# Kernel optimization log

Hardware: AMD Instinct MI355X
Metric: run time of the kernel (lower is better)

## Reference

```python
import jax, jax.numpy as jnp
import numpy as np

N, L, C, KF = 32, 1024, 3, 256
H = C * KF            # hidden_dim = 768
M = 3072              # mlp_dim
EPS = 1e-6


def setup_inputs() -> dict:
    key = jax.random.key(0)
    ks = jax.random.split(key, 14)
    s = lambda fan: 1.0 / np.sqrt(fan)
    return {
        "x": jax.random.normal(ks[0], (N, L, H), dtype=jnp.float32),
        # per-channel QKV linears: Linear(k_factor, 3*k_factor) for each channel
        "W_qkv": jax.random.normal(ks[1], (C, KF, 3 * KF), dtype=jnp.float32) * s(KF),
        "b_qkv": jax.random.normal(ks[2], (C, 3 * KF), dtype=jnp.float32) * 0.01,
        "W_out": jax.random.normal(ks[3], (KF, KF), dtype=jnp.float32) * s(KF),
        "b_out": jax.random.normal(ks[4], (KF,), dtype=jnp.float32) * 0.01,
        "ln1_g": jnp.ones((H,), jnp.float32),
        "ln1_b": jnp.zeros((H,), jnp.float32),
        "ln2_g": jnp.ones((H,), jnp.float32),
        "ln2_b": jnp.zeros((H,), jnp.float32),
        "W1": jax.random.normal(ks[5], (H, M), dtype=jnp.float32) * s(H),
        "b1": jax.random.normal(ks[6], (M,), dtype=jnp.float32) * 1e-6,
        "W2": jax.random.normal(ks[7], (M, H), dtype=jnp.float32) * s(M),
        "b2": jax.random.normal(ks[8], (H,), dtype=jnp.float32) * 1e-6,
    }


def _ln(x, g, b):
    mu = jnp.mean(x, axis=-1, keepdims=True)
    var = jnp.mean(jnp.square(x - mu), axis=-1, keepdims=True)
    return (x - mu) * jax.lax.rsqrt(var + EPS) * g + b


def _criss_cross_attn(h, W_qkv, b_qkv, W_out, b_out):
    # h: [N, L, H]; hidden layout is channel-major: (C, KF)
    hc = h.reshape(h.shape[0], h.shape[1], C, KF)
    qkv = jnp.einsum("nlck,ckd->nlcd", hc, W_qkv) + b_qkv      # [N,L,C,3KF]
    q, k, v = jnp.split(qkv, 3, axis=-1)                        # each [N,L,C,KF]
    # move k_factor axis before channel axis: [N,L,KF,C]
    q = jnp.swapaxes(q, -1, -2)
    k = jnp.swapaxes(k, -1, -2)
    v = jnp.swapaxes(v, -1, -2)
    # outer-product scores over channels: [N,L,KF,C,C]
    scores = q[..., :, None] * k[..., None, :] / np.sqrt(KF)
    attn = jax.nn.softmax(scores, axis=-1)
    # einsum 'ijklm,ijkl->ijkm': sum over first channel axis
    ctx = jnp.einsum("nlkcd,nlkc->nlkd", attn, v)               # [N,L,KF,C]
    ctx = jnp.swapaxes(ctx, -1, -2)                             # [N,L,C,KF]
    out = ctx @ W_out + b_out                                   # fc_out per k_factor
    return out.reshape(h.shape[0], h.shape[1], H)


def reference(x, W_qkv, b_qkv, W_out, b_out, ln1_g, ln1_b, ln2_g, ln2_b, W1, b1, W2, b2):
    h = _ln(x, ln1_g, ln1_b)
    a = _criss_cross_attn(h, W_qkv, b_qkv, W_out, b_out)
    xr = a + x                                                   # residual (dropout=0)
    y = _ln(xr, ln2_g, ln2_b)
    y = jax.nn.gelu(y @ W1 + b1, approximate=False) @ W2 + b2    # MLPBlock
    return xr + y
```

## Files before the change

### kernel.cpp

```cpp
#include <hip/hip_runtime.h>
#include <hip/hip_bf16.h>
#include <math.h>

typedef __attribute__((ext_vector_type(8))) short short8;
typedef __attribute__((ext_vector_type(4))) float f32x4;

__device__ __forceinline__ float bf2f(__hip_bfloat16 h) { return __bfloat162float(h); }
__device__ __forceinline__ __hip_bfloat16 f2bf(float f) { return __float2bfloat16(f); }

__device__ __forceinline__ float gelu_f(float v) {
  const float u = v * (0.7978845608f + 0.0356774081f * v * v);
  const float e = __expf(2.0f * u);
  const float t = 1.0f - 2.0f * __builtin_amdgcn_rcpf(e + 1.0f);
  return 0.5f * v * (1.0f + t);
}

__global__ __launch_bounds__(256) void ln_kernel(
    const float* __restrict__ in, const float* __restrict__ g,
    const float* __restrict__ b, __hip_bfloat16* __restrict__ out)
{
  __shared__ float sm1[4], sm2[4];
  const int row = blockIdx.x;
  const int tid = threadIdx.x;
  const float* p = in + (size_t)row * 768;
  float x0 = p[tid], x1 = p[tid + 256], x2 = p[tid + 512];
  float s = x0 + x1 + x2;
  #pragma unroll
  for (int off = 32; off > 0; off >>= 1) s += __shfl_down(s, off, 64);
  const int l = tid & 63, w = tid >> 6;
  if (l == 0) sm1[w] = s;
  __syncthreads();
  const float mu = (sm1[0] + sm1[1] + sm1[2] + sm1[3]) * (1.0f / 768.0f);
  const float d0 = x0 - mu, d1 = x1 - mu, d2 = x2 - mu;
  float ss = d0*d0 + d1*d1 + d2*d2;
  #pragma unroll
  for (int off = 32; off > 0; off >>= 1) ss += __shfl_down(ss, off, 64);
  if (l == 0) sm2[w] = ss;
  __syncthreads();
  const float var = (sm2[0] + sm2[1] + sm2[2] + sm2[3]) * (1.0f / 768.0f);
  const float rstd = rsqrtf(var + 1e-6f);
  __hip_bfloat16* q = out + (size_t)row * 768;
  q[tid]       = f2bf(d0 * rstd * g[tid]       + b[tid]);
  q[tid + 256] = f2bf(d1 * rstd * g[tid + 256] + b[tid + 256]);
  q[tid + 512] = f2bf(d2 * rstd * g[tid + 512] + b[tid + 512]);
}

__global__ __launch_bounds__(256) void attn_kernel(
    const __hip_bfloat162* __restrict__ qkv, __hip_bfloat162* __restrict__ ctx)
{
  const long t = (long)blockIdx.x * 256 + threadIdx.x;
  const long row = t >> 7;
  const int kp = (int)(t & 127);
  const __hip_bfloat162* p = qkv + row * 1152;
  float q[3][2], k[3][2], v[3][2];
  #pragma unroll
  for (int c = 0; c < 3; ++c) {
    __hip_bfloat162 qq = p[c*384 + kp];
    __hip_bfloat162 kk = p[c*384 + 128 + kp];
    __hip_bfloat162 vv = p[c*384 + 256 + kp];
    q[c][0] = __low2float(qq); q[c][1] = __high2float(qq);
    k[c][0] = __low2float(kk); k[c][1] = __high2float(kk);
    v[c][0] = __low2float(vv); v[c][1] = __high2float(vv);
  }
  float o[3][2] = {};
  #pragma unroll
  for (int u = 0; u < 2; ++u) {
    #pragma unroll
    for (int c = 0; c < 3; ++c) {
      const float s0 = q[c][u]*k[0][u]*0.0625f, s1 = q[c][u]*k[1][u]*0.0625f, s2 = q[c][u]*k[2][u]*0.0625f;
      const float m = fmaxf(s0, fmaxf(s1, s2));
      const float e0 = __expf(s0-m), e1 = __expf(s1-m), e2 = __expf(s2-m);
      const float inv = v[c][u] / (e0 + e1 + e2);
      o[0][u] += e0*inv; o[1][u] += e1*inv; o[2][u] += e2*inv;
    }
  }
  __hip_bfloat162* po = ctx + row * 384;
  #pragma unroll
  for (int d = 0; d < 3; ++d)
    po[d*128 + kp] = __hip_bfloat162{f2bf(o[d][0]), f2bf(o[d][1])};
}

__global__ __launch_bounds__(256) void transpose_bf16_kernel(
    const float* __restrict__ in, __hip_bfloat16* __restrict__ out, int K, int N)
{
  __shared__ float tile[32][33];
  in  += (size_t)blockIdx.z * K * N;
  out += (size_t)blockIdx.z * K * N;
  const int n0 = blockIdx.x * 32;
  const int k0 = blockIdx.y * 32;
  const int tx = threadIdx.x & 31, ty = threadIdx.x >> 5;
  #pragma unroll
  for (int r = 0; r < 32; r += 8)
    tile[ty + r][tx] = in[(size_t)(k0 + ty + r) * N + n0 + tx];
  __syncthreads();
  #pragma unroll
  for (int r = 0; r < 32; r += 8)
    out[(size_t)(n0 + ty + r) * K + k0 + tx] = f2bf(tile[tx][ty + r]);
}

#define BM 128
#define BN 128
#define BK 32

template<int MODE>
__global__ __launch_bounds__(256) void gemm_bt_kernel(
    const __hip_bfloat16* __restrict__ A, int lda, long strideA,
    const __hip_bfloat16* __restrict__ Bt, int ldb, long strideB,
    float* __restrict__ Cf, __hip_bfloat16* __restrict__ Cb, int ldc, long strideC,
    const float* __restrict__ bias, long strideBias,
    const float* __restrict__ res,
    int K)
{
  __shared__ __align__(16) char sAll[2 * 16384];

  const int z = blockIdx.z;
  A    += (size_t)z * strideA;
  Bt   += (size_t)z * strideB;
  bias += (size_t)z * strideBias;
  const long cOff = (long)z * strideC;

  const long tileM = (long)blockIdx.x * BM;
  const int  tileN = blockIdx.y * BN;

  const int tid  = threadIdx.x;
  const int lane = tid & 63;
  const int wv   = tid >> 6;
  const int waveM = (wv & 1) * 64;
  const int waveN = (wv >> 1) * 64;

  const int srow  = tid >> 2;
  const int selem = ((tid & 3) ^ ((srow >> 1) & 3)) * 8;
  const int frow = lane & 15;
  const int fkb  = (((lane >> 4) ^ ((frow >> 1) & 3)) << 4);

  const __hip_bfloat16* Ab = A  + tileM * (size_t)lda + selem;
  const __hip_bfloat16* Bb = Bt + (long)tileN * (size_t)ldb + selem;

  f32x4 acc[4][4] = {};

  const int T = K / BK;

  {
    #pragma unroll
    for (int hh = 0; hh < 2; ++hh) {
      const int r = hh * 64 + srow;
      __builtin_amdgcn_global_load_lds(
          (const __attribute__((address_space(1))) void*)(Ab + (size_t)r * lda),
          (__attribute__((address_space(3))) void*)(sAll + hh*4096 + tid*16), 16, 0, 0);
      __builtin_amdgcn_global_load_lds(
          (const __attribute__((address_space(1))) void*)(Bb + (size_t)r * ldb),
          (__attribute__((address_space(3))) void*)(sAll + 8192 + hh*4096 + tid*16), 16, 0, 0);
    }
  }

  for (int t = 0; t < T; ++t) {
    const int buf = (t & 1) * 16384;
    if (t + 1 < T) {
      const int nbuf = 16384 - buf;
      const int k0 = (t + 1) * BK;
      #pragma unroll
      for (int hh = 0; hh < 2; ++hh) {
        const int r = hh * 64 + srow;
        __builtin_amdgcn_global_load_lds(
            (const __attribute__((address_space(1))) void*)(Ab + (size_t)r * lda + k0),
            (__attribute__((address_space(3))) void*)(sAll + nbuf + hh*4096 + tid*16), 16, 0, 0);
        __builtin_amdgcn_global_load_lds(
            (const __attribute__((address_space(1))) void*)(Bb + (size_t)r * ldb + k0),
            (__attribute__((address_space(3))) void*)(sAll + nbuf + 8192 + hh*4096 + tid*16), 16, 0, 0);
      }
      asm volatile("s_waitcnt vmcnt(4)" ::: "memory");
    } else {
      asm volatile("s_waitcnt vmcnt(0)" ::: "memory");
    }
    __builtin_amdgcn_s_barrier();
    asm volatile("" ::: "memory");

    const char* sAb = sAll + buf;
    const char* sBb = sAb + 8192;
    short8 aF[4], bF[4];
    #pragma unroll
    for (int i = 0; i < 4; ++i)
      aF[i] = *(const short8*)(sAb + (waveM + i*16 + frow) * 64 + fkb);
    #pragma unroll
    for (int j = 0; j < 4; ++j)
      bF[j] = *(const short8*)(sBb + (waveN + j*16 + frow) * 64 + fkb);
    #pragma unroll
    for (int i = 0; i < 4; ++i)
      #pragma unroll
      for (int j = 0; j < 4; ++j)
        acc[i][j] = __builtin_amdgcn_mfma_f32_16x16x32_bf16(aF[i], bF[j], acc[i][j], 0, 0, 0);

    __builtin_amdgcn_s_barrier();
  }

  #pragma unroll
  for (int i = 0; i < 4; ++i) {
    const long row0 = tileM + waveM + i*16 + ((lane >> 4) * 4);
    #pragma unroll
    for (int j = 0; j < 4; ++j) {
      const int col = tileN + waveN + j*16 + (lane & 15);
      const float bv = bias[col];
      #pragma unroll
      for (int r = 0; r < 4; ++r) {
        const long idx = cOff + (row0 + r) * (long)ldc + col;
        const float v = acc[i][j][r] + bv;
        if (MODE == 0) {
          Cb[idx] = f2bf(v);
        } else if (MODE == 1 || MODE == 3) {
          Cf[idx] = v + res[idx];
        } else {
          Cb[idx] = f2bf(gelu_f(v));
        }
      }
    }
  }
}

#define GLL16(src, dst) __builtin_amdgcn_global_load_lds( \
    (const __attribute__((address_space(1))) void*)(src), \
    (__attribute__((address_space(3))) void*)(dst), 16, 0, 0)

#define STAGE_TILE3(bb, koff) do { \
    char* bse = sAll + (bb) * 49152; \
    GLL16(Ab + (size_t)(0*64) * lda + (koff), bse + 0*8192  + tid*16); \
    GLL16(Ab + (size_t)(1*64) * lda + (koff), bse + 1*8192  + tid*16); \
    GLL16(Ab + (size_t)(2*64) * lda + (koff), bse + 2*8192  + tid*16); \
    GLL16(Ab + (size_t)(3*64) * lda + (koff), bse + 3*8192  + tid*16); \
    GLL16(Bb + (size_t)(0*64) * ldb + (koff), bse + 32768 + 0*8192 + tid*16); \
    GLL16(Bb + (size_t)(1*64) * ldb + (koff), bse + 32768 + 1*8192 + tid*16); \
  } while (0)

template<int MODE>
__global__ __launch_bounds__(512, 2) void gemm3_kernel(
    const __hip_bfloat16* __restrict__ A, int lda, long strideA,
    const __hip_bfloat16* __restrict__ Bt, int ldb, long strideB,
    float* __restrict__ Cf, __hip_bfloat16* __restrict__ Cb, int ldc, long strideC,
    const float* __restrict__ bias, long strideBias,
    const float* __restrict__ res,
    int K)
{
  __shared__ __align__(16) char sAll[3 * 49152];

  const int z = blockIdx.z;
  A    += (size_t)z * strideA;
  Bt   += (size_t)z * strideB;
  bias += (size_t)z * strideBias;
  const long cOff = (long)z * strideC;

  const long tileM = (long)blockIdx.x * 256;
  const int  tileN = blockIdx.y * 128;

  const int tid  = threadIdx.x;
  const int lane = tid & 63;
  const int wv   = tid >> 6;
  const int wm   = wv & 3;
  const int wn   = wv >> 2;

  const int srow  = tid >> 3;
  const int selem = ((tid & 7) ^ (srow & 7)) * 8;

  const __hip_bfloat16* Ab = A  + (tileM + srow) * (size_t)lda + selem;
  const __hip_bfloat16* Bb = Bt + ((long)tileN + srow) * (size_t)ldb + selem;

  const int fk   = lane >> 4;
  const int fx   = lane & 7;
  const int frow = lane & 15;
  const int arow = (wm*64 + frow) * 128;
  const int brow = 32768 + (wn*64 + frow) * 128;
  const int ax0  = ((0*4 + fk) ^ fx) * 16;
  const int ax1  = ((1*4 + fk) ^ fx) * 16;

  f32x4 acc[4][4] = {};
  const int T = K / 64;

  STAGE_TILE3(0, 0);
  STAGE_TILE3(1, (T > 1 ? 1 : 0) * 64);

  int bcur = 0;
  for (int t = 0; t < T; ++t) {
    const char* base = sAll + bcur * 49152;
    const int bstg = (bcur == 0) ? 2 : (bcur - 1);
    const int kn   = (t + 2 < T ? t + 2 : T - 1) * 64;

    asm volatile("s_waitcnt vmcnt(6)" ::: "memory");
    __builtin_amdgcn_s_barrier();
    asm volatile("" ::: "memory");

    STAGE_TILE3(bstg, kn);

    short8 aF0[4], bF0[4], aF1[4], bF1[4];
    #pragma unroll
    for (int i = 0; i < 4; ++i) aF0[i] = *(const short8*)(base + arow + i*2048 + ax0);
    #pragma unroll
    for (int j = 0; j < 4; ++j) bF0[j] = *(const short8*)(base + brow + j*2048 + ax0);
    #pragma unroll
    for (int i = 0; i < 4; ++i) aF1[i] = *(const short8*)(base + arow + i*2048 + ax1);
    #pragma unroll
    for (int j = 0; j < 4; ++j) bF1[j] = *(const short8*)(base + brow + j*2048 + ax1);

    asm volatile("s_waitcnt lgkmcnt(8)" ::: "memory");
    __builtin_amdgcn_sched_barrier(0);
    __builtin_amdgcn_s_setprio(1);
    #pragma unroll
    for (int i = 0; i < 4; ++i)
      #pragma unroll
      for (int j = 0; j < 4; ++j)
        acc[i][j] = __builtin_amdgcn_mfma_f32_16x16x32_bf16(aF0[i], bF0[j], acc[i][j], 0, 0, 0);
    __builtin_amdgcn_s_setprio(0);

    asm volatile("s_waitcnt lgkmcnt(0)" ::: "memory");
    __builtin_amdgcn_sched_barrier(0);
    __builtin_amdgcn_s_setprio(1);
    #pragma unroll
    for (int i = 0; i < 4; ++i)
      #pragma unroll
      for (int j = 0; j < 4; ++j)
        acc[i][j] = __builtin_amdgcn_mfma_f32_16x16x32_bf16(aF1[i], bF1[j], acc[i][j], 0, 0, 0);
    __builtin_amdgcn_s_setprio(0);

    bcur = (bcur == 2) ? 0 : (bcur + 1);
  }

  asm volatile("s_waitcnt vmcnt(0)" ::: "memory");

  #pragma unroll
  for (int i = 0; i < 4; ++i) {
    const long row0 = tileM + wm*64 + i*16 + ((lane >> 4) * 4);
    #pragma unroll
    for (int j = 0; j < 4; ++j) {
      const int col = tileN + wn*64 + j*16 + (lane & 15);
      const float bv = bias[col];
      #pragma unroll
      for (int r = 0; r < 4; ++r) {
        const long idx = cOff + (row0 + r) * (long)ldc + col;
        const float v = acc[i][j][r] + bv;
        if (MODE == 0) {
          Cb[idx] = f2bf(v);
        } else if (MODE == 1 || MODE == 3) {
          Cf[idx] = v + res[idx];
        } else {
          Cb[idx] = f2bf(gelu_f(v));
        }
      }
    }
  }
}

extern "C" void kernel_launch(void* const* d_in, const int* in_sizes, int n_in,
                              void* d_out, int out_size, void* d_ws, size_t ws_size,
                              hipStream_t stream)
{
  const float* x     = (const float*)d_in[0];
  const float* W_qkv = (const float*)d_in[1];
  const float* b_qkv = (const float*)d_in[2];
  const float* W_out = (const float*)d_in[3];
  const float* b_out = (const float*)d_in[4];
  const float* ln1_g = (const float*)d_in[5];
  const float* ln1_b = (const float*)d_in[6];
  const float* ln2_g = (const float*)d_in[7];
  const float* ln2_b = (const float*)d_in[8];
  const float* W1    = (const float*)d_in[9];
  const float* b1    = (const float*)d_in[10];
  const float* W2    = (const float*)d_in[11];
  const float* b2    = (const float*)d_in[12];
  float* out = (float*)d_out;

  char* ws = (char*)d_ws;
  __hip_bfloat16* h     = (__hip_bfloat16*)(ws + 0);
  __hip_bfloat16* qkv   = (__hip_bfloat16*)(ws + 50331648);
  __hip_bfloat16* ctx   = (__hip_bfloat16*)(ws + 0);
  __hip_bfloat16* act   = (__hip_bfloat16*)(ws + 0);
  __hip_bfloat16* yln   = (__hip_bfloat16*)(ws + 201326592);
  __hip_bfloat16* wqkvT = (__hip_bfloat16*)(ws + 251658240);
  __hip_bfloat16* woutT = (__hip_bfloat16*)(ws + 252837888);
  __hip_bfloat16* w1T   = (__hip_bfloat16*)(ws + 252968960);
  __hip_bfloat16* w2T   = (__hip_bfloat16*)(ws + 257687552);

  transpose_bf16_kernel<<<dim3(768/32, 256/32, 3), 256, 0, stream>>>(W_qkv, wqkvT, 256, 768);
  transpose_bf16_kernel<<<dim3(256/32, 256/32, 1), 256, 0, stream>>>(W_out, woutT, 256, 256);
  transpose_bf16_kernel<<<dim3(3072/32, 768/32, 1), 256, 0, stream>>>(W1, w1T, 768, 3072);
  transpose_bf16_kernel<<<dim3(768/32, 3072/32, 1), 256, 0, stream>>>(W2, w2T, 3072, 768);

  ln_kernel<<<32768, 256, 0, stream>>>(x, ln1_g, ln1_b, h);

  gemm3_kernel<0><<<dim3(32768/256, 768/128, 3), 512, 0, stream>>>(
      h, 768, 256, wqkvT, 256, 768*256, nullptr, qkv, 2304, 768, b_qkv, 768, nullptr, 256);

  attn_kernel<<<16384, 256, 0, stream>>>((const __hip_bfloat162*)qkv, (__hip_bfloat162*)ctx);

  gemm_bt_kernel<1><<<dim3(98304/BM, 256/BN, 1), 256, 0, stream>>>(
      ctx, 256, 0, woutT, 256, 0, out, nullptr, 256, 0, b_out, 0, x, 256);

  ln_kernel<<<32768, 256, 0, stream>>>(out, ln2_g, ln2_b, yln);

  gemm3_kernel<2><<<dim3(32768/256, 3072/128, 1), 512, 0, stream>>>(
      yln, 768, 0, w1T, 768, 0, nullptr, act, 3072, 0, b1, 0, nullptr, 768);

  gemm3_kernel<3><<<dim3(32768/256, 768/128, 1), 512, 0, stream>>>(
      act, 3072, 0, w2T, 3072, 0, out, nullptr, 768, 0, b2, 0, out, 3072);
}
```

Baseline: 855.5 us.

## Load B fragments directly to registers and enlarge GEMM tile to 256x256

Replaces the 256x128 GEMM with a 256x256-tile kernel. Only A goes through a triple-buffered LDS pipeline; each wave loads its B fragments straight from global memory into double-buffered registers one k-step ahead. The aim is to halve A re-reads across N tiles and to drop LDS traffic for B. In exchange, register use (accumulators plus two B buffers) rises sharply at 2 blocks per CU, the grid shrinks (e.g. only 384 blocks for the 768-wide GEMMs), and uncoalesced direct global B loads may expose latency. The main loop steps two k-tiles per iteration, so odd T would overrun.

```diff
diff --git a/kernel.cpp b/kernel.cpp
--- a/kernel.cpp
+++ b/kernel.cpp
@@ -220,18 +220,76 @@
     (const __attribute__((address_space(1))) void*)(src), \
     (__attribute__((address_space(3))) void*)(dst), 16, 0, 0)
 
-#define STAGE_TILE3(bb, koff) do { \
-    char* bse = sAll + (bb) * 49152; \
-    GLL16(Ab + (size_t)(0*64) * lda + (koff), bse + 0*8192  + tid*16); \
-    GLL16(Ab + (size_t)(1*64) * lda + (koff), bse + 1*8192  + tid*16); \
-    GLL16(Ab + (size_t)(2*64) * lda + (koff), bse + 2*8192  + tid*16); \
-    GLL16(Ab + (size_t)(3*64) * lda + (koff), bse + 3*8192  + tid*16); \
-    GLL16(Bb + (size_t)(0*64) * ldb + (koff), bse + 32768 + 0*8192 + tid*16); \
-    GLL16(Bb + (size_t)(1*64) * ldb + (koff), bse + 32768 + 1*8192 + tid*16); \
+#define STAGE_A3(bb, koff) do { \
+    char* bse = sA3 + (bb) * 32768; \
+    GLL16(Ab + (size_t)(0*64) * lda + (koff), bse + 0*8192 + tid*16); \
+    GLL16(Ab + (size_t)(1*64) * lda + (koff), bse + 1*8192 + tid*16); \
+    GLL16(Ab + (size_t)(2*64) * lda + (koff), bse + 2*8192 + tid*16); \
+    GLL16(Ab + (size_t)(3*64) * lda + (koff), bse + 3*8192 + tid*16); \
   } while (0)
 
+#define LOADB_ALL(dst, kt) do { \
+    _Pragma("unroll") \
+    for (int jh_ = 0; jh_ < 2; ++jh_) \
+      _Pragma("unroll") \
+      for (int j_ = 0; j_ < 2; ++j_) \
+        _Pragma("unroll") \
+        for (int kk_ = 0; kk_ < 2; ++kk_) \
+          dst[jh_][j_][kk_] = *(const short8*)(Bb + (size_t)(jh_*128 + j_*16) * ldb + (kt)*64 + kk_*32); \
+  } while (0)
+
+#define GBODY(t_, bufi, BCUR, BNXT, stg) do { \
+    const char* base = sA3 + (bufi) * 32768; \
+    asm volatile("s_waitcnt vmcnt(4)" ::: "memory");      \
+    __builtin_amdgcn_s_barrier();                         \
+    asm volatile("" ::: "memory"); \
+    short8 aF[4][2]; \
+    _Pragma("unroll") \
+    for (int i_ = 0; i_ < 4; ++i_) { \
+      aF[i_][0] = *(const short8*)(base + arow + i_*2048 + ax0); \
+      aF[i_][1] = *(const short8*)(base + arow + i_*2048 + ax1); \
+    } \
+    { const int ktn = ((t_) + 1 < T ? (t_) + 1 : T - 1); \
+      LOADB_ALL(BNXT, ktn); } \
+    __builtin_amdgcn_sched_barrier(0);                    \
+    { const int kts = ((t_) + 2 < T ? (t_) + 2 : T - 1); \
+      STAGE_A3(stg, kts * 64); } \
+    __builtin_amdgcn_sched_barrier(0); \
+    asm volatile("s_waitcnt lgkmcnt(0)" ::: "memory");    \
+    __builtin_amdgcn_sched_barrier(0); \
+    __builtin_amdgcn_s_setprio(1); \
+    _Pragma("unroll") \
+    for (int i_ = 0; i_ < 4; ++i_) \
+      _Pragma("unroll") \
+      for (int jh_ = 0; jh_ < 2; ++jh_) \
+        _Pragma("unroll") \
+        for (int j_ = 0; j_ < 2; ++j_) { \
+          acc[0][jh_][i_][j_] = __builtin_amdgcn_mfma_f32_16x16x32_bf16(aF[i_][0], BCUR[jh_][j_][0], acc[0][jh_][i_][j_], 0, 0, 0); \
+          acc[0][jh_][i_][j_] = __builtin_amdgcn_mfma_f32_16x16x32_bf16(aF[i_][1], BCUR[jh_][j_][1], acc[0][jh_][i_][j_], 0, 0, 0); \
+        } \
+    __builtin_amdgcn_s_setprio(0); \
+    _Pragma("unroll") \
+    for (int i_ = 0; i_ < 4; ++i_) { \
+      aF[i_][0] = *(const short8*)(base + 16384 + arow + i_*2048 + ax0); \
+      aF[i_][1] = *(const short8*)(base + 16384 + arow + i_*2048 + ax1); \
+    } \
+    asm volatile("s_waitcnt lgkmcnt(0)" ::: "memory");    \
+    __builtin_amdgcn_sched_barrier(0); \
+    __builtin_amdgcn_s_setprio(1); \
+    _Pragma("unroll") \
+    for (int i_ = 0; i_ < 4; ++i_) \
+      _Pragma("unroll") \
+      for (int jh_ = 0; jh_ < 2; ++jh_) \
+        _Pragma("unroll") \
+        for (int j_ = 0; j_ < 2; ++j_) { \
+          acc[1][jh_][i_][j_] = __builtin_amdgcn_mfma_f32_16x16x32_bf16(aF[i_][0], BCUR[jh_][j_][0], acc[1][jh_][i_][j_], 0, 0, 0); \
+          acc[1][jh_][i_][j_] = __builtin_amdgcn_mfma_f32_16x16x32_bf16(aF[i_][1], BCUR[jh_][j_][1], acc[1][jh_][i_][j_], 0, 0, 0); \
+        } \
+    __builtin_amdgcn_s_setprio(0); \
+  } while (0)
+
 template<int MODE>
-__global__ __launch_bounds__(512, 2) void gemm3_kernel(
+__global__ __launch_bounds__(512, 2) void gemmbd_kernel(
     const __hip_bfloat16* __restrict__ A, int lda, long strideA,
     const __hip_bfloat16* __restrict__ Bt, int ldb, long strideB,
     float* __restrict__ Cf, __hip_bfloat16* __restrict__ Cb, int ldc, long strideC,
@@ -239,7 +297,7 @@
     const float* __restrict__ res,
     int K)
 {
-  __shared__ __align__(16) char sAll[3 * 49152];
+  __shared__ __align__(16) char sA3[3 * 32768];
 
   const int z = blockIdx.z;
   A    += (size_t)z * strideA;
@@ -248,102 +306,74 @@
   const long cOff = (long)z * strideC;
 
   const long tileM = (long)blockIdx.x * 256;
-  const int  tileN = blockIdx.y * 128;
+  const int  tileN = blockIdx.y * 256;
 
   const int tid  = threadIdx.x;
   const int lane = tid & 63;
   const int wv   = tid >> 6;
-  const int wm   = wv & 3;
-  const int wn   = wv >> 2;
+  const int wm   = wv & 1;
+  const int wn   = wv >> 1;
 
   const int srow  = tid >> 3;
   const int selem = ((tid & 7) ^ (srow & 7)) * 8;
 
-  const __hip_bfloat16* Ab = A  + (tileM + srow) * (size_t)lda + selem;
-  const __hip_bfloat16* Bb = Bt + ((long)tileN + srow) * (size_t)ldb + selem;
+  const __hip_bfloat16* Ab = A + (tileM + srow) * (size_t)lda + selem;
+
+  const __hip_bfloat16* Bb = Bt + (size_t)(tileN + wn*32 + (lane & 15)) * ldb + ((lane >> 4) * 8);
 
   const int fk   = lane >> 4;
   const int fx   = lane & 7;
   const int frow = lane & 15;
   const int arow = (wm*64 + frow) * 128;
-  const int brow = 32768 + (wn*64 + frow) * 128;
   const int ax0  = ((0*4 + fk) ^ fx) * 16;
   const int ax1  = ((1*4 + fk) ^ fx) * 16;
 
-  f32x4 acc[4][4] = {};
+  f32x4 acc[2][2][4][2] = {};
+  short8 bA[2][2][2], bB[2][2][2];
   const int T = K / 64;
 
-  STAGE_TILE3(0, 0);
-  STAGE_TILE3(1, (T > 1 ? 1 : 0) * 64);
-
-  int bcur = 0;
-  for (int t = 0; t < T; ++t) {
-    const char* base = sAll + bcur * 49152;
-    const int bstg = (bcur == 0) ? 2 : (bcur - 1);
-    const int kn   = (t + 2 < T ? t + 2 : T - 1) * 64;
-
-    asm volatile("s_waitcnt vmcnt(6)" ::: "memory");
-    __builtin_amdgcn_s_barrier();
-    asm volatile("" ::: "memory");
-
-    STAGE_TILE3(bstg, kn);
-
-    short8 aF0[4], bF0[4], aF1[4], bF1[4];
-    #pragma unroll
-    for (int i = 0; i < 4; ++i) aF0[i] = *(const short8*)(base + arow + i*2048 + ax0);
-    #pragma unroll
-    for (int j = 0; j < 4; ++j) bF0[j] = *(const short8*)(base + brow + j*2048 + ax0);
-    #pragma unroll
-    for (int i = 0; i < 4; ++i) aF1[i] = *(const short8*)(base + arow + i*2048 + ax1);
-    #pragma unroll
-    for (int j = 0; j < 4; ++j) bF1[j] = *(const short8*)(base + brow + j*2048 + ax1);
-
-    asm volatile("s_waitcnt lgkmcnt(8)" ::: "memory");
-    __builtin_amdgcn_sched_barrier(0);
-    __builtin_amdgcn_s_setprio(1);
-    #pragma unroll
-    for (int i = 0; i < 4; ++i)
+  STAGE_A3(0, 0);
+  __builtin_amdgcn_sched_barrier(0);
+  LOADB_ALL(bA, 0);
+  __builtin_amdgcn_sched_barrier(0);
+  STAGE_A3(1, (T > 1 ? 1 : 0) * 64);
+
+  int c0 = 0;
+  for (int t = 0; t < T; t += 2) {
+    const int c1 = (c0 + 1 == 3) ? 0 : c0 + 1;
+    const int c2 = (c1 + 1 == 3) ? 0 : c1 + 1;
+    GBODY(t,     c0, bA, bB, c2);
+    GBODY(t + 1, c1, bB, bA, c0);
+    c0 = c2;
+  }
+
+  asm volatile("s_waitcnt vmcnt(0)" ::: "memory");
+
+  #pragma unroll
+  for (int ih = 0; ih < 2; ++ih)
+    #pragma unroll
+    for (int jh = 0; jh < 2; ++jh)
       #pragma unroll
-      for (int j = 0; j < 4; ++j)
-        acc[i][j] = __builtin_amdgcn_mfma_f32_16x16x32_bf16(aF0[i], bF0[j], acc[i][j], 0, 0, 0);
-    __builtin_amdgcn_s_setprio(0);
-
-    asm volatile("s_waitcnt lgkmcnt(0)" ::: "memory");
-    __builtin_amdgcn_sched_barrier(0);
-    __builtin_amdgcn_s_setprio(1);
-    #pragma unroll
-    for (int i = 0; i < 4; ++i)
-      #pragma unroll
-      for (int j = 0; j < 4; ++j)
-        acc[i][j] = __builtin_amdgcn_mfma_f32_16x16x32_bf16(aF1[i], bF1[j], acc[i][j], 0, 0, 0);
-    __builtin_amdgcn_s_setprio(0);
-
-    bcur = (bcur == 2) ? 0 : (bcur + 1);
-  }
-
-  asm volatile("s_waitcnt vmcnt(0)" ::: "memory");
-
-  #pragma unroll
-  for (int i = 0; i < 4; ++i) {
-    const long row0 = tileM + wm*64 + i*16 + ((lane >> 4) * 4);
-    #pragma unroll
-    for (int j = 0; j < 4; ++j) {
-      const int col = tileN + wn*64 + j*16 + (lane & 15);
-      const float bv = bias[col];
-      #pragma unroll
-      for (int r = 0; r < 4; ++r) {
-        const long idx = cOff + (row0 + r) * (long)ldc + col;
-        const float v = acc[i][j][r] + bv;
-        if (MODE == 0) {
-          Cb[idx] = f2bf(v);
-        } else if (MODE == 1 || MODE == 3) {
-          Cf[idx] = v + res[idx];
-        } else {
-          Cb[idx] = f2bf(gelu_f(v));
+      for (int i = 0; i < 4; ++i) {
+        const long row0 = tileM + ih*128 + wm*64 + i*16 + ((lane >> 4) * 4);
+        #pragma unroll
+        for (int j = 0; j < 2; ++j) {
+          const int col = tileN + jh*128 + wn*32 + j*16 + (lane & 15);
+          const float bv = bias[col];
+          #pragma unroll
+          for (int r = 0; r < 4; ++r) {
+            const long idx = cOff + (row0 + r) * (long)ldc + col;
+            const float v = acc[ih][jh][i][j][r] + bv;
+            if (MODE == 0) {
+              Cb[idx] = f2bf(v);
+            } else if (MODE == 1 || MODE == 3) {
+              Cf[idx] = v + res[idx];
+            } else {
+              Cb[idx] = f2bf(gelu_f(v));
+            }
+          }
         }
       }
-    }
-  }
 }
 
 extern "C" void kernel_launch(void* const* d_in, const int* in_sizes, int n_in,
@@ -383,7 +413,7 @@
 
   ln_kernel<<<32768, 256, 0, stream>>>(x, ln1_g, ln1_b, h);
 
-  gemm3_kernel<0><<<dim3(32768/256, 768/128, 3), 512, 0, stream>>>(
+  gemmbd_kernel<0><<<dim3(32768/256, 768/256, 3), 512, 0, stream>>>(
       h, 768, 256, wqkvT, 256, 768*256, nullptr, qkv, 2304, 768, b_qkv, 768, nullptr, 256);
 
   attn_kernel<<<16384, 256, 0, stream>>>((const __hip_bfloat162*)qkv, (__hip_bfloat162*)ctx);
@@ -393,9 +423,9 @@
 
   ln_kernel<<<32768, 256, 0, stream>>>(out, ln2_g, ln2_b, yln);
 
-  gemm3_kernel<2><<<dim3(32768/256, 3072/128, 1), 512, 0, stream>>>(
+  gemmbd_kernel<2><<<dim3(32768/256, 3072/256, 1), 512, 0, stream>>>(
       yln, 768, 0, w1T, 768, 0, nullptr, act, 3072, 0, b1, 0, nullptr, 768);
 
-  gemm3_kernel<3><<<dim3(32768/256, 768/128, 1), 512, 0, stream>>>(
+  gemmbd_kernel<3><<<dim3(32768/256, 768/256, 1), 512, 0, stream>>>(
       act, 3072, 0, w2T, 3072, 0, out, nullptr, 768, 0, b2, 0, out, 3072);
 }
```

Measured after the change: 1.015 ms. 1.19x slower.
